# Kernel tuning notes

Hardware: AMD Instinct MI355X
Metric: run time of the kernel (lower is better)

## Reference

```python
import jax, jax.numpy as jnp
import numpy as np

N = 50000   # nodes
E = 800000  # edges
D = 64      # d_in = d_h = d_out
H1 = 8      # GAT layer-1 heads


def _self_loops(src, dst, n):
    loop = jnp.arange(n)
    return jnp.concatenate([src, loop]), jnp.concatenate([dst, loop])


def gcn_conv(x, src, dst, W, b):
    # PyG GCNConv: symmetric normalization with self-loops, bias added last.
    n = x.shape[0]
    h = x @ W
    s, d = _self_loops(src, dst, n)
    deg = jax.ops.segment_sum(jnp.ones(s.shape[0], h.dtype), d, num_segments=n)
    dinv = jnp.where(deg > 0, deg ** -0.5, 0.0)
    norm = dinv[s] * dinv[d]                                   # [E+N]
    out = jax.ops.segment_sum(h[s] * norm[:, None], d, num_segments=n)
    return out + b


def sage_conv(x, src, dst, Wl, bl, Wr):
    # PyG SAGEConv: mean neighbor aggregation -> lin_l, plus root -> lin_r.
    n = x.shape[0]
    msg = jax.ops.segment_sum(x[src], dst, num_segments=n)
    cnt = jax.ops.segment_sum(jnp.ones(src.shape[0], x.dtype), dst, num_segments=n)
    mean = msg / jnp.maximum(cnt, 1.0)[:, None]
    return mean @ Wl + bl + x @ Wr


def gat_conv(x, src, dst, W, a_src, a_dst, b, heads):
    # PyG GATConv: per-head additive attention, self-loops, segment softmax, concat.
    n = x.shape[0]
    h = (x @ W).reshape(n, heads, -1)                          # [N,H,C]
    al_s = (h * a_src).sum(-1)                                 # [N,H]
    al_d = (h * a_dst).sum(-1)                                 # [N,H]
    s, d = _self_loops(src, dst, n)
    e = jax.nn.leaky_relu(al_s[s] + al_d[d], 0.2)              # [E',H]
    emax = jax.ops.segment_max(e, d, num_segments=n)           # [N,H]
    ex = jnp.exp(e - emax[d])
    den = jax.ops.segment_sum(ex, d, num_segments=n)
    alpha = ex / (den[d] + 1e-16)                              # [E',H]
    out = jax.ops.segment_sum(h[s] * alpha[:, :, None], d, num_segments=n)
    return out.reshape(n, -1) + b


def relu_res(h):
    # get_hiddens: rh = h before ReLU module, then h = relu(h) + rh
    return jax.nn.relu(h) + h


def layer_norm(x, g, b, eps=1e-6):
    mu = x.mean(-1, keepdims=True)
    var = ((x - mu) ** 2).mean(-1, keepdims=True)
    return (x - mu) * jax.lax.rsqrt(var + eps) * g + b


def setup_inputs():
    key = jax.random.key(0)
    ks = jax.random.split(key, 16)
    sc = 1.0 / np.sqrt(D)
    return {
        "x": jax.random.normal(ks[0], (N, D), jnp.float32),
        "edge_index": jax.random.randint(ks[1], (2, E), 0, N),
        "batch": jnp.sort(jax.random.randint(ks[2], (N,), 0, 64)),
        "gcn_W": jax.random.normal(ks[3], (3, D, D), jnp.float32) * sc,
        "gcn_b": jnp.zeros((3, D), jnp.float32),
        "sage_Wl": jax.random.normal(ks[4], (3, D, D), jnp.float32) * sc,
        "sage_bl": jnp.zeros((3, D), jnp.float32),
        "sage_Wr": jax.random.normal(ks[5], (3, D, D), jnp.float32) * sc,
        "gat1_W": jax.random.normal(ks[6], (D, D), jnp.float32) * sc,
        "gat1_asrc": jax.random.normal(ks[7], (H1, D // H1), jnp.float32) * sc,
        "gat1_adst": jax.random.normal(ks[8], (H1, D // H1), jnp.float32) * sc,
        "gat1_b": jnp.zeros((D,), jnp.float32),
        "gat2_W": jax.random.normal(ks[9], (D, D), jnp.float32) * sc,
        "gat2_asrc": jax.random.normal(ks[10], (1, D), jnp.float32) * sc,
        "gat2_adst": jax.random.normal(ks[11], (1, D), jnp.float32) * sc,
        "gat2_b": jnp.zeros((D,), jnp.float32),
        "ln_g": jnp.ones((D,), jnp.float32),
        "ln_b": jnp.zeros((D,), jnp.float32),
    }


def reference(x, edge_index, batch, gcn_W, gcn_b, sage_Wl, sage_bl, sage_Wr,
              gat1_W, gat1_asrc, gat1_adst, gat1_b,
              gat2_W, gat2_asrc, gat2_adst, gat2_b, ln_g, ln_b):
    src, dst = edge_index[0], edge_index[1]
    # channel 0: sz_l=3 GCNConv stack
    h = x
    for l in range(3):
        h = relu_res(gcn_conv(h, src, dst, gcn_W[l], gcn_b[l]))
    c_gcn = h
    # channel 1: GAT(8 heads) -> GAT(1 head)
    h = relu_res(gat_conv(x, src, dst, gat1_W, gat1_asrc, gat1_adst, gat1_b, H1))
    h = relu_res(gat_conv(h, src, dst, gat2_W, gat2_asrc, gat2_adst, gat2_b, 1))
    c_gat = h
    # channel 2: sz_l=3 SAGEConv stack
    h = x
    for l in range(3):
        h = relu_res(sage_conv(h, src, dst, sage_Wl[l], sage_bl[l], sage_Wr[l]))
    c_sage = h
    channal = jnp.stack([c_gcn, c_gat, c_sage])                # [3,N,d_out]
    out = layer_norm(channal, ln_g, ln_b)
    batchs = jnp.ones((3, batch.shape[0]), jnp.float32) * batch.astype(jnp.float32)
    return out, batchs
```

## Files before the change

kernel.cpp:

```cpp
#include <hip/hip_runtime.h>
#include <hip/hip_bf16.h>

typedef __hip_bfloat16 bf16;

static inline int ceil_div(long long a, int b) { return (int)((a + b - 1) / b); }

__device__ __forceinline__ float ld(const void* p, long long i, int f32) {
    return f32 ? ((const float*)p)[i] : __bfloat162float(((const bf16*)p)[i]);
}
__device__ __forceinline__ void st_out(void* p, long long i, int f32, float v) {
    if (f32) ((float*)p)[i] = v;
    else ((bf16*)p)[i] = __float2bfloat16(v);
}
__device__ __forceinline__ float lrelu(float v) { return v > 0.f ? v : 0.2f * v; }

__device__ __forceinline__ float4 f4z() { return make_float4(0.f, 0.f, 0.f, 0.f); }
__device__ __forceinline__ float4 f4add(float4 a, float4 b) {
    return make_float4(a.x + b.x, a.y + b.y, a.z + b.z, a.w + b.w);
}
__device__ __forceinline__ float4 f4fmas(float4 acc, float s, float4 v) {
    return make_float4(fmaf(s, v.x, acc.x), fmaf(s, v.y, acc.y),
                       fmaf(s, v.z, acc.z), fmaf(s, v.w, acc.w));
}
__device__ __forceinline__ float4 f4sxpe(float4 acc, float s, float e, float4 v) {
    return make_float4(fmaf(acc.x, s, e * v.x), fmaf(acc.y, s, e * v.y),
                       fmaf(acc.z, s, e * v.z), fmaf(acc.w, s, e * v.w));
}

__device__ __forceinline__ float4 ldrow4(const void* p, long long row, int c4, int f32) {
    if (f32) return ((const float4*)p)[row * 16 + (c4 >> 2)];
    unsigned long long u = *(const unsigned long long*)((const bf16*)p + row * 64 + c4);
    float4 r;
    r.x = __uint_as_float((unsigned)(u & 0xffffull) << 16);
    r.y = __uint_as_float((unsigned)((u >> 16) & 0xffffull) << 16);
    r.z = __uint_as_float((unsigned)((u >> 32) & 0xffffull) << 16);
    r.w = __uint_as_float((unsigned)(u >> 48) << 16);
    return r;
}

__device__ __forceinline__ int at_idx(int k, int r) {
    return k * 64 + ((((r >> 2) ^ (k & 15)) << 2) | (r & 3));
}

__global__ void k_flag(const void* ln_g, int* flag) {
    if (threadIdx.x == 0)
        flag[0] = (((const unsigned*)ln_g)[0] == 0x3F800000u) ? 1 : 0;
}

__global__ void k_zero_int(int* __restrict__ p, int cnt) {
    int i = blockIdx.x * blockDim.x + threadIdx.x;
    if (i < cnt) p[i] = 0;
}

__global__ void k_count(const int* __restrict__ ei, int E, int* __restrict__ icnt) {
    int e = blockIdx.x * blockDim.x + threadIdx.x;
    if (e < E) atomicAdd(&icnt[ei[E + e]], 1);
}

__global__ void k_scan_blk(const int* __restrict__ icnt, int n,
                           int* __restrict__ local, int* __restrict__ bsum) {
    __shared__ int sh[256];
    int t = threadIdx.x;
    int i = blockIdx.x * 256 + t;
    int c = (i < n) ? icnt[i] : 0;
    sh[t] = c;
    __syncthreads();
    for (int o = 1; o < 256; o <<= 1) {
        int u = (t >= o) ? sh[t - o] : 0;
        __syncthreads();
        sh[t] += u;
        __syncthreads();
    }
    if (i < n) local[i] = sh[t] - c;
    if (t == 255) bsum[blockIdx.x] = sh[255];
}

__global__ void k_scan_top(int* __restrict__ bsum, int nb) {
    __shared__ int sh[256];
    int t = threadIdx.x;
    int c = (t < nb) ? bsum[t] : 0;
    sh[t] = c;
    __syncthreads();
    for (int o = 1; o < 256; o <<= 1) {
        int u = (t >= o) ? sh[t - o] : 0;
        __syncthreads();
        sh[t] += u;
        __syncthreads();
    }
    if (t < nb) bsum[t] = sh[t] - c;
}

__global__ void k_scan_add(int* __restrict__ start, const int* __restrict__ bsum,
                           const int* __restrict__ icnt, float* __restrict__ dinv,
                           float* __restrict__ invc, int n, int E) {
    int i = blockIdx.x * blockDim.x + threadIdx.x;
    if (i < n) {
        start[i] += bsum[i >> 8];
        float fc = (float)icnt[i];
        dinv[i] = rsqrtf(fc + 1.0f);
        invc[i] = 1.0f / fmaxf(fc, 1.0f);
    }
    if (i == 0) start[n] = E;
}

__global__ void k_fill(const int* __restrict__ ei, int E, const int* __restrict__ start,
                       int* __restrict__ cursor, int* __restrict__ csr) {
    int e = blockIdx.x * blockDim.x + threadIdx.x;
    if (e >= E) return;
    int s = ei[e], d = ei[E + e];
    int p = atomicAdd(&cursor[d], 1);
    csr[start[d] + p] = s;
}


__global__ void k_gather12(const void* __restrict__ X,
                           const int* __restrict__ start, const int* __restrict__ csr,
                           const float* __restrict__ dinv, const float* __restrict__ invc,
                           float* __restrict__ Msage, float* __restrict__ Ggcn,
                           int n, const int* __restrict__ flag) {
    int t = threadIdx.x;
    int lane = t & 63, seg = lane >> 4, l16 = lane & 15;
    long long wave = (long long)blockIdx.x * 4 + (t >> 6);
    int d = (int)(wave * 4 + seg);
    if (d >= n) return;
    int xf32 = flag[0];
    int c4 = l16 << 2;
    int s0 = start[d], s1 = start[d + 1];
    float4 a0 = f4z(), a1 = f4z(), g0 = f4z(), g1 = f4z();
    int i = s0;
    for (; i + 3 < s1; i += 4) {
        int sA = csr[i], sB = csr[i + 1], sC = csr[i + 2], sD = csr[i + 3];
        float4 vA = ldrow4(X, sA, c4, xf32);
        float4 vB = ldrow4(X, sB, c4, xf32);
        float4 vC = ldrow4(X, sC, c4, xf32);
        float4 vD = ldrow4(X, sD, c4, xf32);
        float wA = dinv[sA], wB = dinv[sB], wC = dinv[sC], wD = dinv[sD];
        a0 = f4add(a0, vA); g0 = f4fmas(g0, wA, vA);
        a1 = f4add(a1, vB); g1 = f4fmas(g1, wB, vB);
        a0 = f4add(a0, vC); g0 = f4fmas(g0, wC, vC);
        a1 = f4add(a1, vD); g1 = f4fmas(g1, wD, vD);
    }
    for (; i < s1; ++i) {
        int sA = csr[i];
        float4 vA = ldrow4(X, sA, c4, xf32);
        a0 = f4add(a0, vA); g0 = f4fmas(g0, dinv[sA], vA);
    }
    float inv = invc[d];
    float4 ms = f4add(a0, a1);
    float4 gg = f4add(g0, g1);
    ms = make_float4(ms.x * inv, ms.y * inv, ms.z * inv, ms.w * inv);
    *(float4*)&Msage[(long long)d * 64 + c4] = ms;
    *(float4*)&Ggcn[(long long)d * 64 + c4] = gg;
}

__global__ void k_sage_gather(const float* __restrict__ S,
                              const int* __restrict__ start, const int* __restrict__ csr,
                              const float* __restrict__ invc, float* __restrict__ M,
                              int n) {
    int t = threadIdx.x;
    int lane = t & 63, seg = lane >> 4, l16 = lane & 15;
    long long wave = (long long)blockIdx.x * 4 + (t >> 6);
    int d = (int)(wave * 4 + seg);
    if (d >= n) return;
    const float4* S4 = (const float4*)S;
    int s0 = start[d], s1 = start[d + 1];
    float4 a0 = f4z(), a1 = f4z();
    int i = s0;
    for (; i + 3 < s1; i += 4) {
        int sA = csr[i], sB = csr[i + 1], sC = csr[i + 2], sD = csr[i + 3];
        float4 vA = S4[(long long)sA * 16 + l16];
        float4 vB = S4[(long long)sB * 16 + l16];
        float4 vC = S4[(long long)sC * 16 + l16];
        float4 vD = S4[(long long)sD * 16 + l16];
        a0 = f4add(a0, f4add(vA, vC));
        a1 = f4add(a1, f4add(vB, vD));
    }
    for (; i < s1; ++i) a0 = f4add(a0, S4[(long long)csr[i] * 16 + l16]);
    float inv = invc[d];
    float4 r = f4add(a0, a1);
    r = make_float4(r.x * inv, r.y * inv, r.z * inv, r.w * inv);
    *(float4*)&M[(long long)d * 64 + (l16 << 2)] = r;
}

__global__ void k_gcn_gather(const float* __restrict__ T, const int* __restrict__ start,
                             const int* __restrict__ csr, const float* __restrict__ dinv,
                             const void* __restrict__ b_b, const void* __restrict__ b_f,
                             float* __restrict__ P, int n, const int* __restrict__ flag,
                             int do_ln, const void* __restrict__ g, const void* __restrict__ bln,
                             void* __restrict__ outbase, long long elem_off) {
    int t = threadIdx.x;
    int lane = t & 63, seg = lane >> 4, l16 = lane & 15;
    long long wave = (long long)blockIdx.x * 4 + (t >> 6);
    int d = (int)(wave * 4 + seg);
    if (d >= n) return;
    int f32 = flag[0];
    const void* b = f32 ? b_f : b_b;
    int c4 = l16 << 2;
    const float4* T4 = (const float4*)T;
    float wd = dinv[d];
    int s0 = start[d], s1 = start[d + 1];
    float4 a0 = f4z(), a1 = f4z();
    int i = s0;
    for (; i + 3 < s1; i += 4) {
        int sA = csr[i], sB = csr[i + 1], sC = csr[i + 2], sD = csr[i + 3];
        float4 vA = T4[(long long)sA * 16 + l16];
        float4 vB = T4[(long long)sB * 16 + l16];
        float4 vC = T4[(long long)sC * 16 + l16];
        float4 vD = T4[(long long)sD * 16 + l16];
        float wA = dinv[sA], wB = dinv[sB], wC = dinv[sC], wD = dinv[sD];
        a0 = f4fmas(a0, wA, vA); a1 = f4fmas(a1, wB, vB);
        a0 = f4fmas(a0, wC, vC); a1 = f4fmas(a1, wD, vD);
    }
    for (; i < s1; ++i) { int sA = csr[i]; a0 = f4fmas(a0, dinv[sA], T4[(long long)sA * 16 + l16]); }
    float4 sm = f4add(a0, a1);
    float4 selfv = T4[(long long)d * 16 + l16];
    float wd2 = wd * wd;
    float v0 = wd * sm.x + wd2 * selfv.x + ld(b, c4 + 0, f32);
    float v1 = wd * sm.y + wd2 * selfv.y + ld(b, c4 + 1, f32);
    float v2 = wd * sm.z + wd2 * selfv.z + ld(b, c4 + 2, f32);
    float v3 = wd * sm.w + wd2 * selfv.w + ld(b, c4 + 3, f32);
    float4 hv = make_float4(fmaxf(v0, 0.f) + v0, fmaxf(v1, 0.f) + v1,
                            fmaxf(v2, 0.f) + v2, fmaxf(v3, 0.f) + v3);
    if (!do_ln) {
        *(float4*)&P[(long long)d * 64 + c4] = hv;
    } else {
        float loc = (hv.x + hv.y) + (hv.z + hv.w);
        for (int o = 1; o < 16; o <<= 1) loc += __shfl_xor(loc, o, 64);
        float mu = loc * (1.0f / 64.0f);
        float dx = hv.x - mu, dy = hv.y - mu, dz = hv.z - mu, dw = hv.w - mu;
        float s2 = (dx * dx + dy * dy) + (dz * dz + dw * dw);
        for (int o = 1; o < 16; o <<= 1) s2 += __shfl_xor(s2, o, 64);
        float rsig = rsqrtf(s2 * (1.0f / 64.0f) + 1e-6f);
        long long o0 = elem_off + (long long)d * 64 + c4;
        st_out(outbase, o0 + 0, f32, dx * rsig * ld(g, c4 + 0, f32) + ld(bln, c4 + 0, f32));
        st_out(outbase, o0 + 1, f32, dy * rsig * ld(g, c4 + 1, f32) + ld(bln, c4 + 1, f32));
        st_out(outbase, o0 + 2, f32, dz * rsig * ld(g, c4 + 2, f32) + ld(bln, c4 + 2, f32));
        st_out(outbase, o0 + 3, f32, dw * rsig * ld(g, c4 + 3, f32) + ld(bln, c4 + 3, f32));
    }
}

__global__ void k_gat_flash(const float* __restrict__ T, const int* __restrict__ start,
                            const int* __restrict__ csr, const float* __restrict__ als,
                            const float* __restrict__ ald, int n, int H, int hshift,
                            const void* __restrict__ b, float* __restrict__ P,
                            const int* __restrict__ flag) {
    int t = threadIdx.x;
    int lane = t & 63, seg = lane >> 4, l16 = lane & 15;
    long long wave = (long long)blockIdx.x * 4 + (t >> 6);
    int d = (int)(wave * 4 + seg);
    if (d >= n) return;
    int f32 = flag[0];
    int c4 = l16 << 2;
    int h = c4 >> hshift;
    const float4* T4 = (const float4*)T;
    float ad = ald[(long long)d * H + h];
    float m = lrelu(als[(long long)d * H + h] + ad);
    float l = 1.0f;
    float4 acc = T4[(long long)d * 16 + l16];
    int s0 = start[d], s1 = start[d + 1];
    int i = s0;
    for (; i + 3 < s1; i += 4) {
        int sA = csr[i], sB = csr[i + 1], sC = csr[i + 2], sD = csr[i + 3];
        float4 vA = T4[(long long)sA * 16 + l16];
        float4 vB = T4[(long long)sB * 16 + l16];
        float4 vC = T4[(long long)sC * 16 + l16];
        float4 vD = T4[(long long)sD * 16 + l16];
        float lA = lrelu(als[(long long)sA * H + h] + ad);
        float lB = lrelu(als[(long long)sB * H + h] + ad);
        float lC = lrelu(als[(long long)sC * H + h] + ad);
        float lD = lrelu(als[(long long)sD * H + h] + ad);
        float mn = fmaxf(m, fmaxf(fmaxf(lA, lB), fmaxf(lC, lD)));
        float sc = __expf(m - mn);
        float eA = __expf(lA - mn), eB = __expf(lB - mn);
        float eC = __expf(lC - mn), eD = __expf(lD - mn);
        l = fmaf(l, sc, (eA + eB) + (eC + eD));
        acc = f4sxpe(acc, sc, eA, vA);
        acc = f4fmas(acc, eB, vB);
        acc = f4fmas(acc, eC, vC);
        acc = f4fmas(acc, eD, vD);
        m = mn;
    }
    for (; i < s1; ++i) {
        int sA = csr[i];
        float4 vA = T4[(long long)sA * 16 + l16];
        float lA = lrelu(als[(long long)sA * H + h] + ad);
        float mn = fmaxf(m, lA);
        float sc = __expf(m - mn);
        float eA = __expf(lA - mn);
        l = fmaf(l, sc, eA);
        acc = f4sxpe(acc, sc, eA, vA);
        m = mn;
    }
    float rden = 1.0f / (l + 1e-16f);
    float v0 = acc.x * rden + ld(b, c4 + 0, f32);
    float v1 = acc.y * rden + ld(b, c4 + 1, f32);
    float v2 = acc.z * rden + ld(b, c4 + 2, f32);
    float v3 = acc.w * rden + ld(b, c4 + 3, f32);
    float4 o = make_float4(fmaxf(v0, 0.f) + v0, fmaxf(v1, 0.f) + v1,
                           fmaxf(v2, 0.f) + v2, fmaxf(v3, 0.f) + v3);
    *(float4*)&P[(long long)d * 64 + c4] = o;
}

__global__ void k_gemm2(const void* __restrict__ in, const void* __restrict__ W_b,
                        const void* __restrict__ W_f, float* __restrict__ out,
                        int nrows, int in_is_ext, const int* __restrict__ flag) {
    __shared__ __align__(16) float At[64 * 64];
    __shared__ __align__(16) float Ws[64 * 64];
    int f32 = flag[0];
    const void* W = f32 ? W_f : W_b;
    int in_f32 = in_is_ext ? f32 : 1;
    int t = threadIdx.x;
    long long R0 = (long long)blockIdx.x * 64;
    for (int i = t; i < 4096; i += 256) Ws[i] = ld(W, i, f32);
    for (int i = t; i < 4096; i += 256) {
        int r = i >> 6, k = i & 63;
        long long gr = R0 + r;
        At[at_idx(k, r)] = (gr < nrows) ? ld(in, gr * 64 + k, in_f32) : 0.f;
    }
    __syncthreads();
    int tr = t & 15, tc = t >> 4;
    float acc[4][4] = {};
#pragma unroll 8
    for (int k = 0; k < 64; ++k) {
        float4 a = *(const float4*)&At[k * 64 + ((tr ^ (k & 15)) << 2)];
        float4 b = *(const float4*)&Ws[k * 64 + (tc << 2)];
        acc[0][0] = fmaf(a.x, b.x, acc[0][0]); acc[0][1] = fmaf(a.x, b.y, acc[0][1]);
        acc[0][2] = fmaf(a.x, b.z, acc[0][2]); acc[0][3] = fmaf(a.x, b.w, acc[0][3]);
        acc[1][0] = fmaf(a.y, b.x, acc[1][0]); acc[1][1] = fmaf(a.y, b.y, acc[1][1]);
        acc[1][2] = fmaf(a.y, b.z, acc[1][2]); acc[1][3] = fmaf(a.y, b.w, acc[1][3]);
        acc[2][0] = fmaf(a.z, b.x, acc[2][0]); acc[2][1] = fmaf(a.z, b.y, acc[2][1]);
        acc[2][2] = fmaf(a.z, b.z, acc[2][2]); acc[2][3] = fmaf(a.z, b.w, acc[2][3]);
        acc[3][0] = fmaf(a.w, b.x, acc[3][0]); acc[3][1] = fmaf(a.w, b.y, acc[3][1]);
        acc[3][2] = fmaf(a.w, b.z, acc[3][2]); acc[3][3] = fmaf(a.w, b.w, acc[3][3]);
    }
#pragma unroll
    for (int i = 0; i < 4; ++i) {
        long long r = R0 + 4 * tr + i;
        if (r < nrows) {
            float4 v = make_float4(acc[i][0], acc[i][1], acc[i][2], acc[i][3]);
            *(float4*)&out[r * 64 + (tc << 2)] = v;
        }
    }
}

__global__ void k_gat_mm(const void* __restrict__ in, const void* __restrict__ W,
                         float* __restrict__ out, int nrows, int in_is_ext,
                         const int* __restrict__ flag,
                         const void* __restrict__ a_src, const void* __restrict__ a_dst,
                         int C, float* __restrict__ als, float* __restrict__ ald) {
    __shared__ __align__(16) float At[64 * 64];
    __shared__ __align__(16) float Ws[64 * 64];
    int f32 = flag[0];
    int in_f32 = in_is_ext ? f32 : 1;
    int t = threadIdx.x;
    long long R0 = (long long)blockIdx.x * 64;
    for (int i = t; i < 4096; i += 256) Ws[i] = ld(W, i, f32);
    for (int i = t; i < 4096; i += 256) {
        int r = i >> 6, k = i & 63;
        long long gr = R0 + r;
        At[at_idx(k, r)] = (gr < nrows) ? ld(in, gr * 64 + k, in_f32) : 0.f;
    }
    __syncthreads();
    int tr = t & 15, tc = t >> 4;
    float acc[4][4] = {};
#pragma unroll 8
    for (int k = 0; k < 64; ++k) {
        float4 a = *(const float4*)&At[k * 64 + ((tr ^ (k & 15)) << 2)];
        float4 b = *(const float4*)&Ws[k * 64 + (tc << 2)];
        acc[0][0] = fmaf(a.x, b.x, acc[0][0]); acc[0][1] = fmaf(a.x, b.y, acc[0][1]);
        acc[0][2] = fmaf(a.x, b.z, acc[0][2]); acc[0][3] = fmaf(a.x, b.w, acc[0][3]);
        acc[1][0] = fmaf(a.y, b.x, acc[1][0]); acc[1][1] = fmaf(a.y, b.y, acc[1][1]);
        acc[1][2] = fmaf(a.y, b.z, acc[1][2]); acc[1][3] = fmaf(a.y, b.w, acc[1][3]);
        acc[2][0] = fmaf(a.z, b.x, acc[2][0]); acc[2][1] = fmaf(a.z, b.y, acc[2][1]);
        acc[2][2] = fmaf(a.z, b.z, acc[2][2]); acc[2][3] = fmaf(a.z, b.w, acc[2][3]);
        acc[3][0] = fmaf(a.w, b.x, acc[3][0]); acc[3][1] = fmaf(a.w, b.y, acc[3][1]);
        acc[3][2] = fmaf(a.w, b.z, acc[3][2]); acc[3][3] = fmaf(a.w, b.w, acc[3][3]);
    }
#pragma unroll
    for (int i = 0; i < 4; ++i) {
        long long r = R0 + 4 * tr + i;
        if (r < nrows) {
            float4 v = make_float4(acc[i][0], acc[i][1], acc[i][2], acc[i][3]);
            *(float4*)&out[r * 64 + (tc << 2)] = v;
        }
    }
    __syncthreads();
#pragma unroll
    for (int i = 0; i < 4; ++i) {
        float4 v = make_float4(acc[i][0], acc[i][1], acc[i][2], acc[i][3]);
        *(float4*)&At[(4 * tr + i) * 64 + (tc << 2)] = v;
    }
    __syncthreads();
    int w = t >> 6, c = t & 63;
    float av = ld(a_src, c, f32);
    float dv = ld(a_dst, c, f32);
    int H = 64 / C;
    for (int rr = 0; rr < 16; ++rr) {
        int rl = (w << 4) + rr;
        float v = At[rl * 64 + c];
        float ps = v * av, pd = v * dv;
        for (int o = 1; o < C; o <<= 1) {
            ps += __shfl_xor(ps, o, 64);
            pd += __shfl_xor(pd, o, 64);
        }
        long long gr = R0 + rl;
        if ((c & (C - 1)) == 0 && gr < nrows) {
            als[gr * H + (c / C)] = ps;
            ald[gr * H + (c / C)] = pd;
        }
    }
}

__global__ void k_gcn_mm1(const float* __restrict__ G, const void* __restrict__ X,
                          const float* __restrict__ dinv,
                          const void* __restrict__ W_b, const void* __restrict__ W_f,
                          const void* __restrict__ b_b, const void* __restrict__ b_f,
                          float* __restrict__ out, int nrows, const int* __restrict__ flag) {
    __shared__ __align__(16) float At[64 * 64];
    __shared__ __align__(16) float Ws[64 * 64];
    int f32 = flag[0];
    const void* W = f32 ? W_f : W_b;
    int t = threadIdx.x;
    long long R0 = (long long)blockIdx.x * 64;
    for (int i = t; i < 4096; i += 256) Ws[i] = ld(W, i, f32);
    for (int i = t; i < 4096; i += 256) {
        int r = i >> 6, k = i & 63;
        long long gr = R0 + r;
        float v = 0.f;
        if (gr < nrows) {
            float wd = dinv[gr];
            v = wd * G[gr * 64 + k] + wd * wd * ld(X, gr * 64 + k, f32);
        }
        At[at_idx(k, r)] = v;
    }
    __syncthreads();
    int tr = t & 15, tc = t >> 4;
    float acc[4][4] = {};
#pragma unroll 8
    for (int k = 0; k < 64; ++k) {
        float4 a = *(const float4*)&At[k * 64 + ((tr ^ (k & 15)) << 2)];
        float4 b = *(const float4*)&Ws[k * 64 + (tc << 2)];
        acc[0][0] = fmaf(a.x, b.x, acc[0][0]); acc[0][1] = fmaf(a.x, b.y, acc[0][1]);
        acc[0][2] = fmaf(a.x, b.z, acc[0][2]); acc[0][3] = fmaf(a.x, b.w, acc[0][3]);
        acc[1][0] = fmaf(a.y, b.x, acc[1][0]); acc[1][1] = fmaf(a.y, b.y, acc[1][1]);
        acc[1][2] = fmaf(a.y, b.z, acc[1][2]); acc[1][3] = fmaf(a.y, b.w, acc[1][3]);
        acc[2][0] = fmaf(a.z, b.x, acc[2][0]); acc[2][1] = fmaf(a.z, b.y, acc[2][1]);
        acc[2][2] = fmaf(a.z, b.z, acc[2][2]); acc[2][3] = fmaf(a.z, b.w, acc[2][3]);
        acc[3][0] = fmaf(a.w, b.x, acc[3][0]); acc[3][1] = fmaf(a.w, b.y, acc[3][1]);
        acc[3][2] = fmaf(a.w, b.z, acc[3][2]); acc[3][3] = fmaf(a.w, b.w, acc[3][3]);
    }
#pragma unroll
    for (int i = 0; i < 4; ++i) {
        long long r = R0 + 4 * tr + i;
        if (r < nrows) {
            float4 v;
            float v0 = acc[i][0] + ld(f32 ? b_f : b_b, (tc << 2) + 0, f32);
            float v1 = acc[i][1] + ld(f32 ? b_f : b_b, (tc << 2) + 1, f32);
            float v2 = acc[i][2] + ld(f32 ? b_f : b_b, (tc << 2) + 2, f32);
            float v3 = acc[i][3] + ld(f32 ? b_f : b_b, (tc << 2) + 3, f32);
            v.x = fmaxf(v0, 0.f) + v0;
            v.y = fmaxf(v1, 0.f) + v1;
            v.z = fmaxf(v2, 0.f) + v2;
            v.w = fmaxf(v3, 0.f) + v3;
            *(float4*)&out[r * 64 + (tc << 2)] = v;
        }
    }
}

__global__ void k_sage_mm(const float* __restrict__ M, const void* __restrict__ Sx,
                          int s_is_ext,
                          const void* __restrict__ Wl_b, const void* __restrict__ Wl_f,
                          const void* __restrict__ Wr_b, const void* __restrict__ Wr_f,
                          const void* __restrict__ bl_b, const void* __restrict__ bl_f,
                          float* __restrict__ out, int nrows, const int* __restrict__ flag,
                          int do_ln, const void* __restrict__ g, const void* __restrict__ bln,
                          void* __restrict__ outbase, long long elem_off) {
    __shared__ __align__(16) float At[64 * 64];
    __shared__ __align__(16) float Ws[64 * 64];
    int f32 = flag[0];
    int sf32 = s_is_ext ? f32 : 1;
    int t = threadIdx.x;
    long long R0 = (long long)blockIdx.x * 64;
    int tr = t & 15, tc = t >> 4;
    float acc[4][4] = {};

    {
        const void* wl = f32 ? Wl_f : Wl_b;
        for (int i = t; i < 4096; i += 256) Ws[i] = ld(wl, i, f32);
        for (int i = t; i < 4096; i += 256) {
            int r = i >> 6, k = i & 63;
            long long gr = R0 + r;
            At[at_idx(k, r)] = (gr < nrows) ? M[gr * 64 + k] : 0.f;
        }
        __syncthreads();
#pragma unroll 8
        for (int k = 0; k < 64; ++k) {
            float4 a = *(const float4*)&At[k * 64 + ((tr ^ (k & 15)) << 2)];
            float4 b = *(const float4*)&Ws[k * 64 + (tc << 2)];
            acc[0][0] = fmaf(a.x, b.x, acc[0][0]); acc[0][1] = fmaf(a.x, b.y, acc[0][1]);
            acc[0][2] = fmaf(a.x, b.z, acc[0][2]); acc[0][3] = fmaf(a.x, b.w, acc[0][3]);
            acc[1][0] = fmaf(a.y, b.x, acc[1][0]); acc[1][1] = fmaf(a.y, b.y, acc[1][1]);
            acc[1][2] = fmaf(a.y, b.z, acc[1][2]); acc[1][3] = fmaf(a.y, b.w, acc[1][3]);
            acc[2][0] = fmaf(a.z, b.x, acc[2][0]); acc[2][1] = fmaf(a.z, b.y, acc[2][1]);
            acc[2][2] = fmaf(a.z, b.z, acc[2][2]); acc[2][3] = fmaf(a.z, b.w, acc[2][3]);
            acc[3][0] = fmaf(a.w, b.x, acc[3][0]); acc[3][1] = fmaf(a.w, b.y, acc[3][1]);
            acc[3][2] = fmaf(a.w, b.z, acc[3][2]); acc[3][3] = fmaf(a.w, b.w, acc[3][3]);
        }
        __syncthreads();
    }
    {
        const void* wr = f32 ? Wr_f : Wr_b;
        for (int i = t; i < 4096; i += 256) Ws[i] = ld(wr, i, f32);
        for (int i = t; i < 4096; i += 256) {
            int r = i >> 6, k = i & 63;
            long long gr = R0 + r;
            At[at_idx(k, r)] = (gr < nrows) ? ld(Sx, gr * 64 + k, sf32) : 0.f;
        }
        __syncthreads();
#pragma unroll 8
        for (int k = 0; k < 64; ++k) {
            float4 a = *(const float4*)&At[k * 64 + ((tr ^ (k & 15)) << 2)];
            float4 b = *(const float4*)&Ws[k * 64 + (tc << 2)];
            acc[0][0] = fmaf(a.x, b.x, acc[0][0]); acc[0][1] = fmaf(a.x, b.y, acc[0][1]);
            acc[0][2] = fmaf(a.x, b.z, acc[0][2]); acc[0][3] = fmaf(a.x, b.w, acc[0][3]);
            acc[1][0] = fmaf(a.y, b.x, acc[1][0]); acc[1][1] = fmaf(a.y, b.y, acc[1][1]);
            acc[1][2] = fmaf(a.y, b.z, acc[1][2]); acc[1][3] = fmaf(a.y, b.w, acc[1][3]);
            acc[2][0] = fmaf(a.z, b.x, acc[2][0]); acc[2][1] = fmaf(a.z, b.y, acc[2][1]);
            acc[2][2] = fmaf(a.z, b.z, acc[2][2]); acc[2][3] = fmaf(a.z, b.w, acc[2][3]);
            acc[3][0] = fmaf(a.w, b.x, acc[3][0]); acc[3][1] = fmaf(a.w, b.y, acc[3][1]);
            acc[3][2] = fmaf(a.w, b.z, acc[3][2]); acc[3][3] = fmaf(a.w, b.w, acc[3][3]);
        }
    }
    const void* bl = f32 ? bl_f : bl_b;
    float bias[4];
#pragma unroll
    for (int j = 0; j < 4; ++j) bias[j] = ld(bl, (tc << 2) + j, f32);
    float vv[4][4];
#pragma unroll
    for (int i = 0; i < 4; ++i)
#pragma unroll
        for (int j = 0; j < 4; ++j) {
            float v = acc[i][j] + bias[j];
            vv[i][j] = fmaxf(v, 0.f) + v;
        }
    if (!do_ln) {
#pragma unroll
        for (int i = 0; i < 4; ++i) {
            long long r = R0 + 4 * tr + i;
            if (r < nrows) {
                float4 v = make_float4(vv[i][0], vv[i][1], vv[i][2], vv[i][3]);
                *(float4*)&out[r * 64 + (tc << 2)] = v;
            }
        }
    } else {
        __syncthreads();
#pragma unroll
        for (int i = 0; i < 4; ++i) {
            float4 v = make_float4(vv[i][0], vv[i][1], vv[i][2], vv[i][3]);
            *(float4*)&At[(4 * tr + i) * 64 + (tc << 2)] = v;
        }
        __syncthreads();
        int w = t >> 6, lane = t & 63;
        for (int rr = 0; rr < 16; ++rr) {
            int rl = (w << 4) + rr;
            float v = At[rl * 64 + lane];
            float sum = v;
            for (int o = 32; o > 0; o >>= 1) sum += __shfl_xor(sum, o, 64);
            float mu = sum * (1.0f / 64.0f);
            float d0 = v - mu;
            float s2 = d0 * d0;
            for (int o = 32; o > 0; o >>= 1) s2 += __shfl_xor(s2, o, 64);
            float y = d0 * rsqrtf(s2 * (1.0f / 64.0f) + 1e-6f) * ld(g, lane, f32)
                    + ld(bln, lane, f32);
            long long grow = R0 + rl;
            if (grow < nrows)
                st_out(outbase, elem_off + grow * 64 + lane, f32, y);
        }
    }
}

__global__ void k_ln(const float* __restrict__ P, const void* __restrict__ g,
                     const void* __restrict__ b, int n, void* __restrict__ outbase,
                     long long elem_off, const int* __restrict__ flag) {
    int gid = blockIdx.x * blockDim.x + threadIdx.x;
    int node = gid >> 6, lane = gid & 63;
    if (node >= n) return;
    int f32 = flag[0];
    float v = P[(long long)node * 64 + lane];
    float sum = v;
    for (int o = 32; o > 0; o >>= 1) sum += __shfl_xor(sum, o, 64);
    float mu = sum * (1.0f / 64.0f);
    float d0 = v - mu;
    float s2 = d0 * d0;
    for (int o = 32; o > 0; o >>= 1) s2 += __shfl_xor(s2, o, 64);
    float var = s2 * (1.0f / 64.0f);
    float y = d0 * rsqrtf(var + 1e-6f) * ld(g, lane, f32) + ld(b, lane, f32);
    st_out(outbase, elem_off + (long long)node * 64 + lane, f32, y);
}

__global__ void k_batchs(const int* __restrict__ batch, int n, void* __restrict__ outbase,
                         long long elem_off, const int* __restrict__ flag) {
    int idx = blockIdx.x * blockDim.x + threadIdx.x;
    if (idx >= 3 * n) return;
    st_out(outbase, elem_off + idx, flag[0], (float)batch[idx % n]);
}

extern "C" void kernel_launch(void* const* d_in, const int* in_sizes, int n_in,
                              void* d_out, int out_size, void* d_ws, size_t ws_size,
                              hipStream_t stream) {
    const void* x       = d_in[0];
    const int*  ei      = (const int*)d_in[1];
    const int*  batch   = (const int*)d_in[2];
    const char* gcn_W   = (const char*)d_in[3];
    const char* gcn_b   = (const char*)d_in[4];
    const char* sage_Wl = (const char*)d_in[5];
    const char* sage_bl = (const char*)d_in[6];
    const char* sage_Wr = (const char*)d_in[7];
    const void* gat1_W  = d_in[8];
    const void* gat1_as = d_in[9];
    const void* gat1_ad = d_in[10];
    const void* gat1_b  = d_in[11];
    const void* gat2_W  = d_in[12];
    const void* gat2_as = d_in[13];
    const void* gat2_ad = d_in[14];
    const void* gat2_b  = d_in[15];
    const void* ln_g    = d_in[16];
    const void* ln_b    = d_in[17];

    const int n = in_sizes[2];
    const int E = in_sizes[1] / 2;
    const size_t ND = (size_t)n * 64;

    float* P    = (float*)d_ws;
    float* T    = P + ND;
    int*   icnt = (int*)(T + ND);
    float* dinv = (float*)(icnt + n);
    float* invc = dinv + n;
    int*   flag = (int*)(invc + n);

    float* Ggcn  = (float*)d_out;
    int* csr_src = (int*)((char*)d_out + ND * 4);
    int* start   = csr_src + E;
    float* als   = (float*)(start + n + 64);
    float* ald   = als + (size_t)n * 8;
    int* bsum    = (int*)als;

    const int B = 256;
    const int gN    = ceil_div(n, B);
    const int gND   = ceil_div((long long)ND, B);
    const int gE    = ceil_div(E, B);
    const int gT64  = ceil_div(n, 64);
    const int gW4   = ceil_div(n, 16);
    const int nb    = ceil_div(n, 256);

    k_flag<<<1, 64, 0, stream>>>(ln_g, flag);

    k_zero_int<<<gN, B, 0, stream>>>(icnt, n);
    k_count<<<gE, B, 0, stream>>>(ei, E, icnt);
    k_scan_blk<<<nb, 256, 0, stream>>>(icnt, n, start, bsum);
    k_scan_top<<<1, 256, 0, stream>>>(bsum, nb);
    k_scan_add<<<gN, B, 0, stream>>>(start, bsum, icnt, dinv, invc, n, E);
    k_zero_int<<<gN, B, 0, stream>>>(icnt, n);
    k_fill<<<gE, B, 0, stream>>>(ei, E, start, icnt, csr_src);

    k_gather12<<<gW4, B, 0, stream>>>(x, start, csr_src, dinv, invc, P, Ggcn, n, flag);

    {
        k_sage_mm<<<gT64, B, 0, stream>>>(P, x, 1,
            sage_Wl, sage_Wl, sage_Wr, sage_Wr, sage_bl, sage_bl, P, n, flag,
            0, ln_g, ln_b, d_out, 0);
        k_sage_gather<<<gW4, B, 0, stream>>>(P, start, csr_src, invc, T, n);
        k_sage_mm<<<gT64, B, 0, stream>>>(T, P, 0,
            sage_Wl + 4096 * 2, sage_Wl + 4096 * 4, sage_Wr + 4096 * 2, sage_Wr + 4096 * 4,
            sage_bl + 64 * 2, sage_bl + 64 * 4, T, n, flag,
            0, ln_g, ln_b, d_out, 0);
        k_sage_gather<<<gW4, B, 0, stream>>>(T, start, csr_src, invc, P, n);
        k_sage_mm<<<gT64, B, 0, stream>>>(P, T, 0,
            sage_Wl + 8192 * 2, sage_Wl + 8192 * 4, sage_Wr + 8192 * 2, sage_Wr + 8192 * 4,
            sage_bl + 128 * 2, sage_bl + 128 * 4, P, n, flag,
            1, ln_g, ln_b, d_out, 2 * (long long)ND);
    }

    k_gcn_mm1<<<gT64, B, 0, stream>>>(Ggcn, x, dinv, gcn_W, gcn_W, gcn_b, gcn_b,
                                      P, n, flag);
    for (int l = 1; l < 3; ++l) {
        const void* W_b = gcn_W + (size_t)l * 4096 * 2;
        const void* W_f = gcn_W + (size_t)l * 4096 * 4;
        const void* b_b = gcn_b + (size_t)l * 64 * 2;
        const void* b_f = gcn_b + (size_t)l * 64 * 4;
        k_gemm2<<<gT64, B, 0, stream>>>(P, W_b, W_f, T, n, 0, flag);
        k_gcn_gather<<<gW4, B, 0, stream>>>(T, start, csr_src, dinv, b_b, b_f, P, n, flag,
                                            (l == 2) ? 1 : 0, ln_g, ln_b, d_out, 0);
    }

    {
        k_gat_mm<<<gT64, B, 0, stream>>>(x, gat1_W, T, n, 1, flag,
                                         gat1_as, gat1_ad, 8, als, ald);
        k_gat_flash<<<gW4, B, 0, stream>>>(T, start, csr_src, als, ald, n, 8, 3,
                                           gat1_b, P, flag);
        k_gat_mm<<<gT64, B, 0, stream>>>(P, gat2_W, T, n, 0, flag,
                                         gat2_as, gat2_ad, 64, als, ald);
        k_gat_flash<<<gW4, B, 0, stream>>>(T, start, csr_src, als, ald, n, 1, 6,
                                           gat2_b, P, flag);
    }
    k_ln<<<gND, B, 0, stream>>>(P, ln_g, ln_b, n, d_out, (long long)ND, flag);

    k_batchs<<<ceil_div((long long)3 * n, B), B, 0, stream>>>(batch, n, d_out,
                                                              3 * (long long)ND, flag);
}
```

Baseline: 657.7 us.

## Build CSR via block-local bucketing and unroll neighbor gathers to eight

The per-edge global-atomic CSR fill is replaced by two passes. The first sorts each 4096-edge chunk in shared memory by 256-node bucket and writes the (src,dst) pairs to a bucketed staging array with coalesced stores. The second scatters each bucket into the CSR using shared-memory cursors. The aim is to avoid scattered global atomics and random writes, at the cost of an extra kernel and staging traffic through the T buffer. The bucket scheme assumes at most 256 buckets, so n must be at most 65536. Separately, all gather and attention loops are unrolled from 4 to 8 neighbors to keep more independent loads in flight.

```diff
diff --git a/kernel.cpp b/kernel.cpp
--- a/kernel.cpp
+++ b/kernel.cpp
@@ -103,13 +103,72 @@
     if (i == 0) start[n] = E;
 }
 
-__global__ void k_fill(const int* __restrict__ ei, int E, const int* __restrict__ start,
-                       int* __restrict__ cursor, int* __restrict__ csr) {
-    int e = blockIdx.x * blockDim.x + threadIdx.x;
-    if (e >= E) return;
-    int s = ei[e], d = ei[E + e];
-    int p = atomicAdd(&cursor[d], 1);
-    csr[start[d] + p] = s;
+__global__ void k_bucket(const int* __restrict__ ei, int E,
+                         const int* __restrict__ start, int* __restrict__ gcur,
+                         int2* __restrict__ se, int n) {
+    __shared__ int2 buf[4096];
+    __shared__ int lcnt[256], loff[256], lcur[256], gb[256], sh[256];
+    int t = threadIdx.x;
+    long long base = (long long)blockIdx.x * 4096;
+    int cnt = (int)(((long long)E - base) < 4096 ? ((long long)E - base) : 4096);
+    lcnt[t] = 0;
+    __syncthreads();
+#pragma unroll
+    for (int it = 0; it < 16; ++it) {
+        int idx = (it << 8) + t;
+        if (idx < cnt) {
+            int d = ei[E + base + idx];
+            atomicAdd(&lcnt[d >> 8], 1);
+        }
+    }
+    __syncthreads();
+    int c = lcnt[t];
+    sh[t] = c;
+    __syncthreads();
+    for (int o = 1; o < 256; o <<= 1) {
+        int u = (t >= o) ? sh[t - o] : 0;
+        __syncthreads();
+        sh[t] += u;
+        __syncthreads();
+    }
+    loff[t] = sh[t] - c;
+    lcur[t] = sh[t] - c;
+    if (c > 0) gb[t] = start[t << 8] + atomicAdd(&gcur[t], c);
+    __syncthreads();
+#pragma unroll
+    for (int it = 0; it < 16; ++it) {
+        int idx = (it << 8) + t;
+        if (idx < cnt) {
+            long long e = base + idx;
+            int s = ei[e], d = ei[E + e];
+            int p = atomicAdd(&lcur[d >> 8], 1);
+            buf[p] = make_int2(s, d);
+        }
+    }
+    __syncthreads();
+    for (int i = t; i < cnt; i += 256) {
+        int2 e = buf[i];
+        int b = e.y >> 8;
+        se[gb[b] + (i - loff[b])] = e;
+    }
+}
+
+__global__ void k_fill2(const int2* __restrict__ se, const int* __restrict__ start,
+                        int* __restrict__ csr, int n) {
+    __shared__ int cur[256];
+    int t = threadIdx.x;
+    int node0 = blockIdx.x << 8;
+    int node = node0 + t;
+    cur[t] = (node < n) ? start[node] : 0;
+    __syncthreads();
+    int nend = node0 + 256; if (nend > n) nend = n;
+    int e0 = start[node0];
+    int e1 = start[nend];
+    for (int i = e0 + t; i < e1; i += 256) {
+        int2 e = se[i];
+        int p = atomicAdd(&cur[e.y & 255], 1);
+        csr[p] = e.x;
+    }
 }
 
 
@@ -128,7 +187,29 @@
     int s0 = start[d], s1 = start[d + 1];
     float4 a0 = f4z(), a1 = f4z(), g0 = f4z(), g1 = f4z();
     int i = s0;
-    for (; i + 3 < s1; i += 4) {
+    for (; i + 7 < s1; i += 8) {
+        int sA = csr[i],     sB = csr[i + 1], sC = csr[i + 2], sD = csr[i + 3];
+        int sE = csr[i + 4], sF = csr[i + 5], sG = csr[i + 6], sH = csr[i + 7];
+        float4 vA = ldrow4(X, sA, c4, xf32);
+        float4 vB = ldrow4(X, sB, c4, xf32);
+        float4 vC = ldrow4(X, sC, c4, xf32);
+        float4 vD = ldrow4(X, sD, c4, xf32);
+        float4 vE = ldrow4(X, sE, c4, xf32);
+        float4 vF = ldrow4(X, sF, c4, xf32);
+        float4 vG = ldrow4(X, sG, c4, xf32);
+        float4 vH = ldrow4(X, sH, c4, xf32);
+        float wA = dinv[sA], wB = dinv[sB], wC = dinv[sC], wD = dinv[sD];
+        float wE = dinv[sE], wF = dinv[sF], wG = dinv[sG], wH = dinv[sH];
+        a0 = f4add(a0, vA); g0 = f4fmas(g0, wA, vA);
+        a1 = f4add(a1, vB); g1 = f4fmas(g1, wB, vB);
+        a0 = f4add(a0, vC); g0 = f4fmas(g0, wC, vC);
+        a1 = f4add(a1, vD); g1 = f4fmas(g1, wD, vD);
+        a0 = f4add(a0, vE); g0 = f4fmas(g0, wE, vE);
+        a1 = f4add(a1, vF); g1 = f4fmas(g1, wF, vF);
+        a0 = f4add(a0, vG); g0 = f4fmas(g0, wG, vG);
+        a1 = f4add(a1, vH); g1 = f4fmas(g1, wH, vH);
+    }
+    if (i + 3 < s1) {
         int sA = csr[i], sB = csr[i + 1], sC = csr[i + 2], sD = csr[i + 3];
         float4 vA = ldrow4(X, sA, c4, xf32);
         float4 vB = ldrow4(X, sB, c4, xf32);
@@ -139,6 +220,7 @@
         a1 = f4add(a1, vB); g1 = f4fmas(g1, wB, vB);
         a0 = f4add(a0, vC); g0 = f4fmas(g0, wC, vC);
         a1 = f4add(a1, vD); g1 = f4fmas(g1, wD, vD);
+        i += 4;
     }
     for (; i < s1; ++i) {
         int sA = csr[i];
@@ -166,7 +248,23 @@
     int s0 = start[d], s1 = start[d + 1];
     float4 a0 = f4z(), a1 = f4z();
     int i = s0;
-    for (; i + 3 < s1; i += 4) {
+    for (; i + 7 < s1; i += 8) {
+        int sA = csr[i],     sB = csr[i + 1], sC = csr[i + 2], sD = csr[i + 3];
+        int sE = csr[i + 4], sF = csr[i + 5], sG = csr[i + 6], sH = csr[i + 7];
+        float4 vA = S4[(long long)sA * 16 + l16];
+        float4 vB = S4[(long long)sB * 16 + l16];
+        float4 vC = S4[(long long)sC * 16 + l16];
+        float4 vD = S4[(long long)sD * 16 + l16];
+        float4 vE = S4[(long long)sE * 16 + l16];
+        float4 vF = S4[(long long)sF * 16 + l16];
+        float4 vG = S4[(long long)sG * 16 + l16];
+        float4 vH = S4[(long long)sH * 16 + l16];
+        a0 = f4add(a0, f4add(vA, vC));
+        a1 = f4add(a1, f4add(vB, vD));
+        a0 = f4add(a0, f4add(vE, vG));
+        a1 = f4add(a1, f4add(vF, vH));
+    }
+    if (i + 3 < s1) {
         int sA = csr[i], sB = csr[i + 1], sC = csr[i + 2], sD = csr[i + 3];
         float4 vA = S4[(long long)sA * 16 + l16];
         float4 vB = S4[(long long)sB * 16 + l16];
@@ -174,6 +272,7 @@
         float4 vD = S4[(long long)sD * 16 + l16];
         a0 = f4add(a0, f4add(vA, vC));
         a1 = f4add(a1, f4add(vB, vD));
+        i += 4;
     }
     for (; i < s1; ++i) a0 = f4add(a0, S4[(long long)csr[i] * 16 + l16]);
     float inv = invc[d];
@@ -201,7 +300,25 @@
     int s0 = start[d], s1 = start[d + 1];
     float4 a0 = f4z(), a1 = f4z();
     int i = s0;
-    for (; i + 3 < s1; i += 4) {
+    for (; i + 7 < s1; i += 8) {
+        int sA = csr[i],     sB = csr[i + 1], sC = csr[i + 2], sD = csr[i + 3];
+        int sE = csr[i + 4], sF = csr[i + 5], sG = csr[i + 6], sH = csr[i + 7];
+        float4 vA = T4[(long long)sA * 16 + l16];
+        float4 vB = T4[(long long)sB * 16 + l16];
+        float4 vC = T4[(long long)sC * 16 + l16];
+        float4 vD = T4[(long long)sD * 16 + l16];
+        float4 vE = T4[(long long)sE * 16 + l16];
+        float4 vF = T4[(long long)sF * 16 + l16];
+        float4 vG = T4[(long long)sG * 16 + l16];
+        float4 vH = T4[(long long)sH * 16 + l16];
+        float wA = dinv[sA], wB = dinv[sB], wC = dinv[sC], wD = dinv[sD];
+        float wE = dinv[sE], wF = dinv[sF], wG = dinv[sG], wH = dinv[sH];
+        a0 = f4fmas(a0, wA, vA); a1 = f4fmas(a1, wB, vB);
+        a0 = f4fmas(a0, wC, vC); a1 = f4fmas(a1, wD, vD);
+        a0 = f4fmas(a0, wE, vE); a1 = f4fmas(a1, wF, vF);
+        a0 = f4fmas(a0, wG, vG); a1 = f4fmas(a1, wH, vH);
+    }
+    if (i + 3 < s1) {
         int sA = csr[i], sB = csr[i + 1], sC = csr[i + 2], sD = csr[i + 3];
         float4 vA = T4[(long long)sA * 16 + l16];
         float4 vB = T4[(long long)sB * 16 + l16];
@@ -210,6 +327,7 @@
         float wA = dinv[sA], wB = dinv[sB], wC = dinv[sC], wD = dinv[sD];
         a0 = f4fmas(a0, wA, vA); a1 = f4fmas(a1, wB, vB);
         a0 = f4fmas(a0, wC, vC); a1 = f4fmas(a1, wD, vD);
+        i += 4;
     }
     for (; i < s1; ++i) { int sA = csr[i]; a0 = f4fmas(a0, dinv[sA], T4[(long long)sA * 16 + l16]); }
     float4 sm = f4add(a0, a1);
@@ -259,7 +377,44 @@
     float4 acc = T4[(long long)d * 16 + l16];
     int s0 = start[d], s1 = start[d + 1];
     int i = s0;
-    for (; i + 3 < s1; i += 4) {
+    for (; i + 7 < s1; i += 8) {
+        int sA = csr[i],     sB = csr[i + 1], sC = csr[i + 2], sD = csr[i + 3];
+        int sE = csr[i + 4], sF = csr[i + 5], sG = csr[i + 6], sH = csr[i + 7];
+        float4 vA = T4[(long long)sA * 16 + l16];
+        float4 vB = T4[(long long)sB * 16 + l16];
+        float4 vC = T4[(long long)sC * 16 + l16];
+        float4 vD = T4[(long long)sD * 16 + l16];
+        float4 vE = T4[(long long)sE * 16 + l16];
+        float4 vF = T4[(long long)sF * 16 + l16];
+        float4 vG = T4[(long long)sG * 16 + l16];
+        float4 vH = T4[(long long)sH * 16 + l16];
+        float lA = lrelu(als[(long long)sA * H + h] + ad);
+        float lB = lrelu(als[(long long)sB * H + h] + ad);
+        float lC = lrelu(als[(long long)sC * H + h] + ad);
+        float lD = lrelu(als[(long long)sD * H + h] + ad);
+        float lE = lrelu(als[(long long)sE * H + h] + ad);
+        float lF = lrelu(als[(long long)sF * H + h] + ad);
+        float lG = lrelu(als[(long long)sG * H + h] + ad);
+        float lH = lrelu(als[(long long)sH * H + h] + ad);
+        float mn = fmaxf(m, fmaxf(fmaxf(fmaxf(lA, lB), fmaxf(lC, lD)),
+                                  fmaxf(fmaxf(lE, lF), fmaxf(lG, lH))));
+        float sc = __expf(m - mn);
+        float eA = __expf(lA - mn), eB = __expf(lB - mn);
+        float eC = __expf(lC - mn), eD = __expf(lD - mn);
+        float eE = __expf(lE - mn), eF = __expf(lF - mn);
+        float eG = __expf(lG - mn), eH = __expf(lH - mn);
+        l = fmaf(l, sc, ((eA + eB) + (eC + eD)) + ((eE + eF) + (eG + eH)));
+        acc = f4sxpe(acc, sc, eA, vA);
+        acc = f4fmas(acc, eB, vB);
+        acc = f4fmas(acc, eC, vC);
+        acc = f4fmas(acc, eD, vD);
+        acc = f4fmas(acc, eE, vE);
+        acc = f4fmas(acc, eF, vF);
+        acc = f4fmas(acc, eG, vG);
+        acc = f4fmas(acc, eH, vH);
+        m = mn;
+    }
+    if (i + 3 < s1) {
         int sA = csr[i], sB = csr[i + 1], sC = csr[i + 2], sD = csr[i + 3];
         float4 vA = T4[(long long)sA * 16 + l16];
         float4 vB = T4[(long long)sB * 16 + l16];
@@ -279,6 +434,7 @@
         acc = f4fmas(acc, eC, vC);
         acc = f4fmas(acc, eD, vD);
         m = mn;
+        i += 4;
     }
     for (; i < s1; ++i) {
         int sA = csr[i];
@@ -637,6 +793,8 @@
     float* dinv = (float*)(icnt + n);
     float* invc = dinv + n;
     int*   flag = (int*)(invc + n);
+    int*   gcur = flag + 64;
+    int2*  se   = (int2*)T;
 
     float* Ggcn  = (float*)d_out;
     int* csr_src = (int*)((char*)d_out + ND * 4);
@@ -660,8 +818,9 @@
     k_scan_blk<<<nb, 256, 0, stream>>>(icnt, n, start, bsum);
     k_scan_top<<<1, 256, 0, stream>>>(bsum, nb);
     k_scan_add<<<gN, B, 0, stream>>>(start, bsum, icnt, dinv, invc, n, E);
-    k_zero_int<<<gN, B, 0, stream>>>(icnt, n);
-    k_fill<<<gE, B, 0, stream>>>(ei, E, start, icnt, csr_src);
+    k_zero_int<<<1, 256, 0, stream>>>(gcur, 256);
+    k_bucket<<<ceil_div(E, 4096), 256, 0, stream>>>(ei, E, start, gcur, se, n);
+    k_fill2<<<nb, 256, 0, stream>>>(se, start, csr_src, n);
 
     k_gather12<<<gW4, B, 0, stream>>>(x, start, csr_src, dinv, invc, P, Ggcn, n, flag);
 
```

Measured after the change: 637.8 us. 3.0% less time.
